# Optimization experiments

Measured on AMD Instinct MI355X. Metric: run time of the kernel, lower is better.

## Reference

```python
import jax, jax.numpy as jnp
import numpy as np

CAPS_N, DIMS_N, ROUNDS = 10, 16, 3
IN_CAPS_N, IN_DIMS_N = 1152, 8
BATCH = 256
EPS = 1e-7  # keras backend.epsilon()


def squash(x, axis=-1):
    sq = jnp.sum(x * x, axis=axis, keepdims=True)
    return (sq / (1.0 + sq)) * x / jnp.sqrt(sq + EPS)


def setup_inputs() -> dict:
    key = jax.random.key(0)
    k1, k2 = jax.random.split(key)
    inputs = jax.random.normal(k1, (BATCH, IN_CAPS_N, IN_DIMS_N), dtype=jnp.float32)
    # glorot-ish scale for the transform weights
    W = jax.random.normal(k2, (CAPS_N, IN_CAPS_N, DIMS_N, IN_DIMS_N), dtype=jnp.float32) * 0.05
    return {"inputs": inputs, "W": W}


def reference(inputs, W):
    # u_hat[b,j,i,d] = W[j,i] @ inputs[b,i]  (per-pair prediction vectors)
    u_hat = jnp.einsum('jide,bie->bjid', W, inputs)  # [B, caps_n, in_caps_n, dims_n]
    B = inputs.shape[0]
    cc = jnp.zeros((B, CAPS_N, IN_CAPS_N), dtype=u_hat.dtype)  # routing logits
    v = None
    for r in range(ROUNDS):
        c = jax.nn.softmax(cc, axis=1)                    # softmax over output capsules
        s = jnp.einsum('bji,bjid->bjd', c, u_hat)         # weighted sum over input caps
        v = squash(s, axis=-1)                            # [B, caps_n, dims_n]
        if r != ROUNDS - 1:
            cc = cc + jnp.einsum('bjid,bjd->bji', u_hat, v)  # agreement
    return v
```

## Files before the change

### kernel.cpp

```cpp
#include <hip/hip_runtime.h>

#define B_N 256
#define IC_N 1152
#define J_N 10
#define D_N 16

typedef __attribute__((ext_vector_type(8))) short short8;
typedef __attribute__((ext_vector_type(4))) float floatx4;

union u4s8 { uint4 u; short8 s; };

__device__ __forceinline__ float bf_lo(unsigned int u){
  union { unsigned int i; float f; } c; c.i = u << 16; return c.f;
}
__device__ __forceinline__ float bf_hi(unsigned int u){
  union { unsigned int i; float f; } c; c.i = u & 0xffff0000u; return c.f;
}
__device__ __forceinline__ unsigned int rne16(float f){
  union { float ff; unsigned int i; } c; c.ff = f;
  return (c.i + 0x7FFFu + ((c.i >> 16) & 1u)) >> 16;
}
__device__ __forceinline__ unsigned int pack_rne(float lo, float hi){
  return rne16(lo) | (rne16(hi) << 16);
}
__device__ __forceinline__ unsigned int pack_trunc(float lo, float hi){
  union { float f; unsigned int u; } a, b; a.f = lo; b.f = hi;
  return __builtin_amdgcn_perm(b.u, a.u, 0x07060302u);
}

__global__ __launch_bounds__(256) void caps_prep(
    const float* __restrict__ W, uint4* __restrict__ wsf,
    uint4* __restrict__ wcc2, float* __restrict__ vsum)
{
  const int tid = threadIdx.x;
  const int t0 = blockIdx.x * 256 + tid;
  if (t0 < B_N * J_N * D_N) vsum[t0] = 0.f;
  __shared__ unsigned int lw[1024];
  const int j = blockIdx.x / 72, itile = blockIdx.x % 72;
  const float4* Wt = (const float4*)(W + ((size_t)(j * IC_N + itile * 16) << 7));
  #pragma unroll
  for (int h = 0; h < 2; ++h) {
    const float4 f = Wt[h * 256 + tid];
    lw[(h * 256 + tid) * 2]     = pack_rne(f.x, f.y);
    lw[(h * 256 + tid) * 2 + 1] = pack_rne(f.z, f.w);
  }
  __syncthreads();
  {
    const int ktl = tid >> 6, ln = tid & 63;
    const int base = (ktl * 4 + (ln >> 4)) * 64 + (ln & 15) * 4;
    uint4 q;
    q.x = lw[base]; q.y = lw[base + 1]; q.z = lw[base + 2]; q.w = lw[base + 3];
    wsf[((size_t)j * 288 + itile * 4 + ktl) * 64 + ln] = q;
  }
  {
    const int e = tid >> 5, lane2 = tid & 31;
    const int il = lane2 & 15, dbase = (lane2 >> 4) * 8;
    unsigned short h[8];
    #pragma unroll
    for (int k = 0; k < 8; ++k) {
      const unsigned int u = lw[il * 64 + (dbase + k) * 4 + (e >> 1)];
      h[k] = (e & 1) ? (unsigned short)(u >> 16) : (unsigned short)(u & 0xffffu);
    }
    uint4 q;
    q.x = h[0] | ((unsigned int)h[1] << 16);
    q.y = h[2] | ((unsigned int)h[3] << 16);
    q.z = h[4] | ((unsigned int)h[5] << 16);
    q.w = h[6] | ((unsigned int)h[7] << 16);
    wcc2[(((size_t)j * 8 + e) * 72 + itile) * 32 + lane2] = q;
  }
}

__global__ __launch_bounds__(320, 5) void caps_pass(
    const float* __restrict__ x,
    const uint4* __restrict__ wsf, const uint4* __restrict__ wcc2,
    const uint4* __restrict__ vsbf, float* __restrict__ s_part, const int round)
{
  __shared__ float ccl[10 * 16 * 17];
  __shared__ unsigned int xt[16 * 17 * 4];

  const int tid  = threadIdx.x;
  const int wave = tid >> 6;
  const int lane = tid & 63;
  const int quad = lane >> 4;
  const int col  = lane & 15;
  const int b0   = blockIdx.x << 4;
  const int i0   = blockIdx.y << 4;

  for (int p = tid; p < 512; p += 320) {
    const int b = p >> 5, u = p & 31, i = u >> 1, half = u & 1;
    const float4 v = ((const float4*)(x + ((size_t)((b0 + b) * IC_N + i0 + i) << 3)))[half];
    const int idx = ((i * 17 + b) << 2) + (half << 1);
    xt[idx]     = pack_rne(v.x, v.y);
    xt[idx + 1] = pack_rne(v.z, v.w);
  }
  __syncthreads();
  const uint4* xtq = (const uint4*)xt;

  if (round > 0) {
    uint4 xr[4];
    #pragma unroll
    for (int r = 0; r < 4; ++r)
      xr[r] = xtq[col * 17 + quad * 4 + r];
    #pragma unroll
    for (int jj = 0; jj < 2; ++jj) {
      const int j = wave * 2 + jj;
      short8 av = {0,0,0,0,0,0,0,0};
      if (quad < 2)
        av = *(const short8*)&vsbf[((size_t)(b0 + col) * J_N + j) * 2 + quad];
      uint4 bvq[8];
      #pragma unroll
      for (int e = 0; e < 8; ++e) {
        uint4 q = {0u, 0u, 0u, 0u};
        if (lane < 32)
          q = wcc2[(((size_t)j * 8 + e) * 72 + blockIdx.y) * 32 + lane];
        bvq[e] = q;
      }
      floatx4 cc4 = {0.f, 0.f, 0.f, 0.f};
      #pragma unroll
      for (int e = 0; e < 8; ++e) {
        u4s8 bv; bv.u = bvq[e];
        floatx4 tf = {0.f, 0.f, 0.f, 0.f};
        tf = __builtin_amdgcn_mfma_f32_16x16x32_bf16(av, bv.s, tf, 0, 0, 0);
        #pragma unroll
        for (int r = 0; r < 4; ++r) {
          const unsigned int u = ((const unsigned int*)&xr[r])[e >> 1];
          const float xe = (e & 1) ? bf_hi(u) : bf_lo(u);
          cc4[r] += tf[r] * xe;
        }
      }
      #pragma unroll
      for (int r = 0; r < 4; ++r)
        ccl[(j * 16 + col) * 17 + quad * 4 + r] = cc4[r];
    }
    __syncthreads();
    if (tid < 256) {
      const int i = tid >> 4, b = tid & 15;
      float cc[10];
      #pragma unroll
      for (int j = 0; j < 10; ++j) cc[j] = ccl[(j * 16 + i) * 17 + b];
      float m = cc[0];
      #pragma unroll
      for (int j = 1; j < 10; ++j) m = fmaxf(m, cc[j]);
      float den = 0.f;
      #pragma unroll
      for (int j = 0; j < 10; ++j) { cc[j] = __expf(cc[j] - m); den += cc[j]; }
      const float rd = __builtin_amdgcn_rcpf(den);
      #pragma unroll
      for (int j = 0; j < 10; ++j) ccl[(j * 16 + i) * 17 + b] = cc[j] * rd;
    }
    __syncthreads();
  }

  #pragma unroll
  for (int jj = 0; jj < 2; ++jj) {
    const int j = wave * 2 + jj;
    floatx4 acc = {0.f, 0.f, 0.f, 0.f};
    #pragma unroll
    for (int kt = 0; kt < 4; ++kt) {
      const int il = kt * 4 + quad;
      const uint4 xq = xtq[il * 17 + col];
      const uint4 wf = wsf[((size_t)j * 288 + (blockIdx.y << 2) + kt) * 64 + lane];
      const float c = (round > 0) ? ccl[(j * 16 + il) * 17 + col] : 0.1f;
      short8 af;
      unsigned int* aq = (unsigned int*)&af;
      aq[0] = pack_trunc(bf_lo(xq.x) * c, bf_hi(xq.x) * c);
      aq[1] = pack_trunc(bf_lo(xq.y) * c, bf_hi(xq.y) * c);
      aq[2] = pack_trunc(bf_lo(xq.z) * c, bf_hi(xq.z) * c);
      aq[3] = pack_trunc(bf_lo(xq.w) * c, bf_hi(xq.w) * c);
      u4s8 bw; bw.u = wf;
      acc = __builtin_amdgcn_mfma_f32_16x16x32_bf16(af, bw.s, acc, 0, 0, 0);
    }
    float* sp = s_part + ((((size_t)blockIdx.x * 10 + j) * 16 + quad * 4) * 72
                          + blockIdx.y) * 16 + col;
    #pragma unroll
    for (int r = 0; r < 4; ++r) sp[(size_t)r * 72 * 16] = acc[r];
  }
}

__global__ __launch_bounds__(256) void caps_squash(
    const float* __restrict__ s_part, float* __restrict__ vsum,
    unsigned int* __restrict__ vsbf_u, float* __restrict__ out, const int round)
{
  const int tid  = threadIdx.x;
  const int w    = tid >> 6;
  const int lane = tid & 63;
  const int bj   = blockIdx.x * 4 + w;
  const int b    = bj / 10, j = bj - b * 10;
  const int btile = b >> 4, brem = b & 15;
  const float* base = s_part + (((size_t)btile * 10 + j) * 16 + brem) * 1152;
  float acc = 0.f;
  #pragma unroll
  for (int q = 0; q < 18; ++q) acc += base[q * 64 + lane];
  acc += __shfl_xor(acc, 16, 64);
  acc += __shfl_xor(acc, 32, 64);
  const float s = acc;
  float sq = s * s;
  sq += __shfl_xor(sq, 1, 16);
  sq += __shfl_xor(sq, 2, 16);
  sq += __shfl_xor(sq, 4, 16);
  sq += __shfl_xor(sq, 8, 16);
  const float coef = (sq / (1.f + sq)) * rsqrtf(sq + 1e-7f);
  const float v = coef * s;
  if (round < 2) {
    const float vprev = (lane < 16) ? vsum[bj * 16 + lane] : 0.f;
    const float vt = vprev + v;
    const float vtn = __shfl_down(vt, 1, 64);
    if (lane < 16) {
      vsum[bj * 16 + lane] = vt;
      if (!(lane & 1))
        vsbf_u[bj * 8 + (lane >> 1)] = pack_rne(vt, vtn);
    }
  } else if (lane < 16) {
    out[bj * 16 + lane] = v;
  }
}

extern "C" void kernel_launch(void* const* d_in, const int* in_sizes, int n_in,
                              void* d_out, int out_size, void* d_ws, size_t ws_size,
                              hipStream_t stream)
{
  const float* x_p = (const float*)d_in[0];
  const float* W_p = (const float*)d_in[1];

  uint4* wsf   = (uint4*)d_ws;
  uint4* wcc2  = wsf + 184320;
  float* s_prt = (float*)(wcc2 + 184320);
  float* vsum  = s_prt + 2949120;
  unsigned int* vsbf_u = (unsigned int*)(vsum + 40960);
  float* out_p = (float*)d_out;

  caps_prep<<<dim3(720), dim3(256), 0, stream>>>(W_p, wsf, wcc2, vsum);
  for (int r = 0; r < 3; ++r) {
    caps_pass<<<dim3(16, 72), dim3(320), 0, stream>>>(
        x_p, wsf, wcc2, (const uint4*)vsbf_u, s_prt, r);
    caps_squash<<<dim3(640), dim3(256), 0, stream>>>(
        s_prt, vsum, vsbf_u, out_p, r);
  }
}
```

Before: 116.9 us.

## Replace partial-sum buffer and squash kernels with atomic accumulation and in-pass squash

```diff
diff --git a/kernel.cpp b/kernel.cpp
--- a/kernel.cpp
+++ b/kernel.cpp
@@ -30,11 +30,11 @@
 
 __global__ __launch_bounds__(256) void caps_prep(
     const float* __restrict__ W, uint4* __restrict__ wsf,
-    uint4* __restrict__ wcc2, float* __restrict__ vsum)
+    uint4* __restrict__ wcc2, float* __restrict__ s_zero)
 {
   const int tid = threadIdx.x;
   const int t0 = blockIdx.x * 256 + tid;
-  if (t0 < B_N * J_N * D_N) vsum[t0] = 0.f;
+  if (t0 < 3 * B_N * J_N * D_N) s_zero[t0] = 0.f;
   __shared__ unsigned int lw[1024];
   const int j = blockIdx.x / 72, itile = blockIdx.x % 72;
   const float4* Wt = (const float4*)(W + ((size_t)(j * IC_N + itile * 16) << 7));
@@ -73,10 +73,12 @@
 __global__ __launch_bounds__(320, 5) void caps_pass(
     const float* __restrict__ x,
     const uint4* __restrict__ wsf, const uint4* __restrict__ wcc2,
-    const uint4* __restrict__ vsbf, float* __restrict__ s_part, const int round)
+    const float* __restrict__ s0, const float* __restrict__ s1,
+    float* __restrict__ s_w, const int round)
 {
   __shared__ float ccl[10 * 16 * 17];
   __shared__ unsigned int xt[16 * 17 * 4];
+  __shared__ unsigned int vsh[160 * 8];
 
   const int tid  = threadIdx.x;
   const int wave = tid >> 6;
@@ -93,6 +95,25 @@
     xt[idx]     = pack_rne(v.x, v.y);
     xt[idx + 1] = pack_rne(v.z, v.w);
   }
+  if (round > 0 && tid < 160) {
+    const int j = tid >> 4, bl = tid & 15;
+    float vacc[16];
+    #pragma unroll
+    for (int d = 0; d < 16; ++d) vacc[d] = 0.f;
+    for (int rr = 0; rr < round; ++rr) {
+      const float* sp = (rr == 0 ? s0 : s1) + ((size_t)(b0 + bl) * 160 + j * 16);
+      float sv[16];
+      float sq = 0.f;
+      #pragma unroll
+      for (int d = 0; d < 16; ++d) { sv[d] = sp[d]; sq += sv[d] * sv[d]; }
+      const float coef = (sq / (1.f + sq)) * rsqrtf(sq + 1e-7f);
+      #pragma unroll
+      for (int d = 0; d < 16; ++d) vacc[d] += coef * sv[d];
+    }
+    #pragma unroll
+    for (int k = 0; k < 8; ++k)
+      vsh[(bl * 10 + j) * 8 + k] = pack_rne(vacc[2 * k], vacc[2 * k + 1]);
+  }
   __syncthreads();
   const uint4* xtq = (const uint4*)xt;
 
@@ -106,7 +127,7 @@
       const int j = wave * 2 + jj;
       short8 av = {0,0,0,0,0,0,0,0};
       if (quad < 2)
-        av = *(const short8*)&vsbf[((size_t)(b0 + col) * J_N + j) * 2 + quad];
+        av = *(const short8*)&vsh[(col * 10 + j) * 8 + quad * 4];
       uint4 bvq[8];
       #pragma unroll
       for (int e = 0; e < 8; ++e) {
@@ -170,49 +191,25 @@
       u4s8 bw; bw.u = wf;
       acc = __builtin_amdgcn_mfma_f32_16x16x32_bf16(af, bw.s, acc, 0, 0, 0);
     }
-    float* sp = s_part + ((((size_t)blockIdx.x * 10 + j) * 16 + quad * 4) * 72
-                          + blockIdx.y) * 16 + col;
-    #pragma unroll
-    for (int r = 0; r < 4; ++r) sp[(size_t)r * 72 * 16] = acc[r];
-  }
-}
-
-__global__ __launch_bounds__(256) void caps_squash(
-    const float* __restrict__ s_part, float* __restrict__ vsum,
-    unsigned int* __restrict__ vsbf_u, float* __restrict__ out, const int round)
-{
-  const int tid  = threadIdx.x;
-  const int w    = tid >> 6;
-  const int lane = tid & 63;
-  const int bj   = blockIdx.x * 4 + w;
-  const int b    = bj / 10, j = bj - b * 10;
-  const int btile = b >> 4, brem = b & 15;
-  const float* base = s_part + (((size_t)btile * 10 + j) * 16 + brem) * 1152;
-  float acc = 0.f;
-  #pragma unroll
-  for (int q = 0; q < 18; ++q) acc += base[q * 64 + lane];
-  acc += __shfl_xor(acc, 16, 64);
-  acc += __shfl_xor(acc, 32, 64);
-  const float s = acc;
+    #pragma unroll
+    for (int r = 0; r < 4; ++r)
+      __hip_atomic_fetch_add(&s_w[(size_t)(b0 + quad * 4 + r) * 160 + j * 16 + col],
+                             acc[r], __ATOMIC_RELAXED, __HIP_MEMORY_SCOPE_AGENT);
+  }
+}
+
+__global__ __launch_bounds__(256) void caps_outsq(
+    const float* __restrict__ s2, float* __restrict__ out)
+{
+  const int t = blockIdx.x * 256 + threadIdx.x;
+  const float s = s2[t];
   float sq = s * s;
   sq += __shfl_xor(sq, 1, 16);
   sq += __shfl_xor(sq, 2, 16);
   sq += __shfl_xor(sq, 4, 16);
   sq += __shfl_xor(sq, 8, 16);
   const float coef = (sq / (1.f + sq)) * rsqrtf(sq + 1e-7f);
-  const float v = coef * s;
-  if (round < 2) {
-    const float vprev = (lane < 16) ? vsum[bj * 16 + lane] : 0.f;
-    const float vt = vprev + v;
-    const float vtn = __shfl_down(vt, 1, 64);
-    if (lane < 16) {
-      vsum[bj * 16 + lane] = vt;
-      if (!(lane & 1))
-        vsbf_u[bj * 8 + (lane >> 1)] = pack_rne(vt, vtn);
-    }
-  } else if (lane < 16) {
-    out[bj * 16 + lane] = v;
-  }
+  out[t] = coef * s;
 }
 
 extern "C" void kernel_launch(void* const* d_in, const int* in_sizes, int n_in,
@@ -222,18 +219,16 @@
   const float* x_p = (const float*)d_in[0];
   const float* W_p = (const float*)d_in[1];
 
-  uint4* wsf   = (uint4*)d_ws;
-  uint4* wcc2  = wsf + 184320;
-  float* s_prt = (float*)(wcc2 + 184320);
-  float* vsum  = s_prt + 2949120;
-  unsigned int* vsbf_u = (unsigned int*)(vsum + 40960);
+  uint4* wsf  = (uint4*)d_ws;
+  uint4* wcc2 = wsf + 184320;
+  float* s0   = (float*)(wcc2 + 184320);
+  float* s1   = s0 + 40960;
+  float* s2   = s1 + 40960;
   float* out_p = (float*)d_out;
 
-  caps_prep<<<dim3(720), dim3(256), 0, stream>>>(W_p, wsf, wcc2, vsum);
-  for (int r = 0; r < 3; ++r) {
-    caps_pass<<<dim3(16, 72), dim3(320), 0, stream>>>(
-        x_p, wsf, wcc2, (const uint4*)vsbf_u, s_prt, r);
-    caps_squash<<<dim3(640), dim3(256), 0, stream>>>(
-        s_prt, vsum, vsbf_u, out_p, r);
-  }
-}
+  caps_prep<<<dim3(720), dim3(256), 0, stream>>>(W_p, wsf, wcc2, s0);
+  caps_pass<<<dim3(16, 72), dim3(320), 0, stream>>>(x_p, wsf, wcc2, s0, s1, s0, 0);
+  caps_pass<<<dim3(16, 72), dim3(320), 0, stream>>>(x_p, wsf, wcc2, s0, s1, s1, 1);
+  caps_pass<<<dim3(16, 72), dim3(320), 0, stream>>>(x_p, wsf, wcc2, s0, s1, s2, 2);
+  caps_outsq<<<dim3(160), dim3(256), 0, stream>>>(s2, out_p);
+}
```

Result: no change. 118.0 us (+0.9%).
